# Performance work log

Hardware: AMD Instinct MI355X
Metric: run time of the kernel (lower is better)

The kernel has to match this reference:

```python
import jax, jax.numpy as jnp
import numpy as np

DEPTH, E, H, S, V, B = 6, 1024, 16, 2048, 32000, 2
HD = E // H
EPS = 1e-5


def _layernorm(x, w, b):
    mu = jnp.mean(x, axis=-1, keepdims=True)
    var = jnp.mean(jnp.square(x - mu), axis=-1, keepdims=True)
    return (x - mu) * jax.lax.rsqrt(var + EPS) * w + b


def setup_inputs() -> dict:
    key = jax.random.key(0)
    ks = jax.random.split(key, 8)
    std = 0.02
    return {
        "idx": jax.random.randint(ks[0], (B, S), 0, V),
        "tok_emb": jax.random.normal(ks[1], (V, E), jnp.float32) * std,
        "pos_emb": jax.random.normal(ks[2], (S, E), jnp.float32) * std,
        "qkv_w": jax.random.normal(ks[3], (DEPTH, 3 * E, E), jnp.float32) * std,
        "qkv_b": jnp.zeros((DEPTH, 3 * E), jnp.float32),
        "ln1_w": jnp.ones((DEPTH, E), jnp.float32),
        "ln1_b": jnp.zeros((DEPTH, E), jnp.float32),
        "ln2_w": jnp.ones((DEPTH, E), jnp.float32),
        "ln2_b": jnp.zeros((DEPTH, E), jnp.float32),
        "ff1_w": jax.random.normal(ks[4], (DEPTH, 4 * E, E), jnp.float32) * std,
        "ff1_b": jnp.zeros((DEPTH, 4 * E), jnp.float32),
        "ff2_w": jax.random.normal(ks[5], (DEPTH, E, 4 * E), jnp.float32) * std,
        "ff2_b": jnp.zeros((DEPTH, E), jnp.float32),
        "fin_w": jnp.ones((E,), jnp.float32),
        "fin_b": jnp.zeros((E,), jnp.float32),
        "proj_w": jax.random.normal(ks[6], (V, E), jnp.float32) * std,
    }


def _block(x, qkv_w, qkv_b, ln1_w, ln1_b, ln2_w, ln2_b, ff1_w, ff1_b, ff2_w, ff2_b):
    bs, seq, _ = x.shape
    # --- causal MSA (dropout in eval mode -> identity) ---
    xn = _layernorm(x, ln1_w, ln1_b)
    qkv = xn @ qkv_w.T + qkv_b                      # [B,S,3E]
    qkv = qkv.reshape(bs, seq, 3, H, HD)
    q, k, v = (jnp.moveaxis(qkv[:, :, i], 1, 2) for i in range(3))  # [B,H,S,HD]
    scores = jnp.einsum("bhqd,bhkd->bhqk", q, k) / jnp.sqrt(jnp.float32(HD))
    causal = jnp.triu(jnp.ones((seq, seq), bool), k=1)
    scores = jnp.where(causal[None, None], -jnp.inf, scores)
    probs = jax.nn.softmax(scores, axis=-1)
    attn = jnp.einsum("bhqk,bhkd->bqhd", probs, v).reshape(bs, seq, E)
    x = x + attn
    # --- feedforward ---
    xn = _layernorm(x, ln2_w, ln2_b)
    h = jax.nn.gelu(xn @ ff1_w.T + ff1_b, approximate=False)
    x = x + (h @ ff2_w.T + ff2_b)
    return x


def reference(idx, tok_emb, pos_emb, qkv_w, qkv_b, ln1_w, ln1_b, ln2_w, ln2_b,
              ff1_w, ff1_b, ff2_w, ff2_b, fin_w, fin_b, proj_w):
    bs, seq = idx.shape
    x = tok_emb[idx] + pos_emb[jnp.arange(seq)][None]  # [B,S,E]
    for l in range(DEPTH):
        x = _block(x, qkv_w[l], qkv_b[l], ln1_w[l], ln1_b[l], ln2_w[l], ln2_b[l],
                   ff1_w[l], ff1_b[l], ff2_w[l], ff2_b[l])
    x = _layernorm(x, fin_w, fin_b)
    logits = x @ proj_w.T  # [B,S,V], final_proj has no bias
    return logits
```

## Files before the change

### kernel.cpp

```cpp
#include <hip/hip_runtime.h>
#include <hip/hip_bf16.h>

#define DEPTH 6
#define E 1024
#define H 16
#define S 2048
#define V 32000
#define BB 2
#define HD 64
#define NTOK (BB * S)

typedef __attribute__((ext_vector_type(8))) short bf16x8;
typedef __attribute__((ext_vector_type(4))) float f32x4;
typedef unsigned short us;

__device__ inline us f2bf(float f) {
    union { float f; unsigned u; } v; v.f = f;
    unsigned r = v.u + 0x7fff + ((v.u >> 16) & 1);
    return (us)(r >> 16);
}
__device__ inline float bf2f(us b) {
    union { unsigned u; float f; } v; v.u = ((unsigned)b) << 16;
    return v.f;
}

__device__ __forceinline__ void gld16(const us* g, us* l) {
    __builtin_amdgcn_global_load_lds(
        (const __attribute__((address_space(1))) unsigned int*)g,
        (__attribute__((address_space(3))) unsigned int*)l, 16, 0, 0);
}

__global__ __launch_bounds__(256) void cast_kernel(const float* __restrict__ in,
                                                   us* __restrict__ out, int n8) {
    int i = blockIdx.x * 256 + threadIdx.x;
    if (i >= n8) return;
    const float4* p = (const float4*)in + 2 * (size_t)i;
    float4 a = p[0], b = p[1];
    uint4 o;
    o.x = f2bf(a.x) | ((unsigned)f2bf(a.y) << 16);
    o.y = f2bf(a.z) | ((unsigned)f2bf(a.w) << 16);
    o.z = f2bf(b.x) | ((unsigned)f2bf(b.y) << 16);
    o.w = f2bf(b.z) | ((unsigned)f2bf(b.w) << 16);
    ((uint4*)out)[i] = o;
}

__global__ void embed_kernel(const int* __restrict__ idx, const float* __restrict__ tok,
                             const float* __restrict__ pos, float* __restrict__ x) {
    int t = blockIdx.x;
    int s = t & (S - 1);
    int tokid = idx[t];
    int c = threadIdx.x * 4;
    float4 a = *(const float4*)&tok[(size_t)tokid * E + c];
    float4 p = *(const float4*)&pos[(size_t)s * E + c];
    float4 o; o.x = a.x + p.x; o.y = a.y + p.y; o.z = a.z + p.z; o.w = a.w + p.w;
    *(float4*)&x[(size_t)t * E + c] = o;
}

__global__ __launch_bounds__(256) void ln_kernel(const float* __restrict__ x,
                                                 const float* __restrict__ w,
                                                 const float* __restrict__ b,
                                                 us* __restrict__ out) {
    int row = blockIdx.x;
    int tid = threadIdx.x;
    int c = tid * 4;
    float4 v = *(const float4*)&x[(size_t)row * E + c];
    float s  = v.x + v.y + v.z + v.w;
    float sq = v.x * v.x + v.y * v.y + v.z * v.z + v.w * v.w;
    __shared__ float red[8];
    for (int o = 32; o > 0; o >>= 1) { s += __shfl_xor(s, o); sq += __shfl_xor(sq, o); }
    int wave = tid >> 6, lane = tid & 63;
    if (lane == 0) { red[wave] = s; red[4 + wave] = sq; }
    __syncthreads();
    if (tid == 0) {
        red[0] = red[0] + red[1] + red[2] + red[3];
        red[4] = red[4] + red[5] + red[6] + red[7];
    }
    __syncthreads();
    float mean = red[0] * (1.0f / E);
    float var  = red[4] * (1.0f / E) - mean * mean;
    float rstd = rsqrtf(var + 1e-5f);
    float4 wv = *(const float4*)&w[c];
    float4 bv = *(const float4*)&b[c];
    unsigned a0 = f2bf((v.x - mean) * rstd * wv.x + bv.x);
    unsigned a1 = f2bf((v.y - mean) * rstd * wv.y + bv.y);
    unsigned a2 = f2bf((v.z - mean) * rstd * wv.z + bv.z);
    unsigned a3 = f2bf((v.w - mean) * rstd * wv.w + bv.w);
    uint2 o; o.x = a0 | (a1 << 16); o.y = a2 | (a3 << 16);
    *(uint2*)&out[(size_t)row * E + c] = o;
}

__global__ __launch_bounds__(256) void combine_ln(const us* __restrict__ p0,
                                                  const us* __restrict__ p1,
                                                  const float* __restrict__ bias,
                                                  float* __restrict__ x,
                                                  const float* __restrict__ w,
                                                  const float* __restrict__ b,
                                                  us* __restrict__ out) {
    int row = blockIdx.x;
    int tid = threadIdx.x;
    int c = tid * 4;
    size_t base = (size_t)row * E + c;
    float4 v = *(const float4*)&x[base];
    uint2 a = *(const uint2*)&p0[base];
    uint2 bb2 = *(const uint2*)&p1[base];
    float4 bi = *(const float4*)&bias[c];
    v.x += bf2f((us)(a.x & 0xffff)) + bf2f((us)(bb2.x & 0xffff)) + bi.x;
    v.y += bf2f((us)(a.x >> 16))    + bf2f((us)(bb2.x >> 16))    + bi.y;
    v.z += bf2f((us)(a.y & 0xffff)) + bf2f((us)(bb2.y & 0xffff)) + bi.z;
    v.w += bf2f((us)(a.y >> 16))    + bf2f((us)(bb2.y >> 16))    + bi.w;
    *(float4*)&x[base] = v;

    float s  = v.x + v.y + v.z + v.w;
    float sq = v.x * v.x + v.y * v.y + v.z * v.z + v.w * v.w;
    __shared__ float red[8];
    for (int o = 32; o > 0; o >>= 1) { s += __shfl_xor(s, o); sq += __shfl_xor(sq, o); }
    int wave = tid >> 6, lane = tid & 63;
    if (lane == 0) { red[wave] = s; red[4 + wave] = sq; }
    __syncthreads();
    if (tid == 0) {
        red[0] = red[0] + red[1] + red[2] + red[3];
        red[4] = red[4] + red[5] + red[6] + red[7];
    }
    __syncthreads();
    float mean = red[0] * (1.0f / E);
    float var  = red[4] * (1.0f / E) - mean * mean;
    float rstd = rsqrtf(var + 1e-5f);
    float4 wv = *(const float4*)&w[c];
    float4 bv = *(const float4*)&b[c];
    unsigned a0 = f2bf((v.x - mean) * rstd * wv.x + bv.x);
    unsigned a1 = f2bf((v.y - mean) * rstd * wv.y + bv.y);
    unsigned a2 = f2bf((v.z - mean) * rstd * wv.z + bv.z);
    unsigned a3 = f2bf((v.w - mean) * rstd * wv.w + bv.w);
    uint2 o; o.x = a0 | (a1 << 16); o.y = a2 | (a3 << 16);
    *(uint2*)&out[base] = o;
}

#define GPH(dd, fb, STAGE, ISVM, IS12)                                              \
  {                                                                                 \
    bf16x8 afr0[2], afr1[2];                                                        \
    if ((fb) == 0) {                                                                \
      _Pragma("unroll")                                                             \
      for (int n = 0; n < 4; n++)                                                   \
        _Pragma("unroll")                                                           \
        for (int ks = 0; ks < 2; ks++)                                              \
          bfr[n][ks] = *(const bf16x8*)&lds[32768 + (dd) * 16384 +                  \
              (brow + n * 16) * 64 + ((ks * 4 + g4) ^ xg) * 8];                     \
    }                                                                               \
    _Pragma("unroll")                                                               \
    for (int ks = 0; ks < 2; ks++) {                                                \
      afr0[ks] = *(const bf16x8*)&lds[(dd) * 16384 + ((fb) >> 1) * 4096 +           \
          arow0 * 64 + ((ks * 4 + g4) ^ xg) * 8];                                   \
      afr1[ks] = *(const bf16x8*)&lds[(dd) * 16384 + ((fb) >> 1) * 4096 +           \
          arow1 * 64 + ((ks * 4 + g4) ^ xg) * 8];                                   \
    }                                                                               \
    STAGE;                                                                          \
    __builtin_amdgcn_sched_barrier(0);                                              \
    if (IS12) asm volatile("s_waitcnt lgkmcnt(8)" ::: "memory");                    \
    __builtin_amdgcn_s_barrier();                                                   \
    asm volatile("s_waitcnt lgkmcnt(0)" ::: "memory");                              \
    __builtin_amdgcn_sched_barrier(0);                                              \
    __builtin_amdgcn_s_setprio(1);                                                  \
    _Pragma("unroll")                                                               \
    for (int n = 0; n < 4; n++)                                                     \
      _Pragma("unroll")                                                             \
      for (int ks = 0; ks < 2; ks++) {                                              \
        acc[(fb)][n]     = __builtin_amdgcn_mfma_f32_16x16x32_bf16(afr0[ks], bfr[n][ks], acc[(fb)][n], 0, 0, 0);     \
        acc[(fb) + 1][n] = __builtin_amdgcn_mfma_f32_16x16x32_bf16(afr1[ks], bfr[n][ks], acc[(fb) + 1][n], 0, 0, 0); \
      }                                                                             \
    __builtin_amdgcn_s_setprio(0);                                                  \
    __builtin_amdgcn_sched_barrier(0);                                              \
    if (ISVM) asm volatile("s_waitcnt vmcnt(6)" ::: "memory");                      \
    __builtin_amdgcn_s_barrier();                                                   \
  }

template <int OUT_BF16, int ACT_GELU, int HAS_BIAS>
__global__ __launch_bounds__(512, 2) void gemm256(const us* __restrict__ A, int lda,
                                                  const us* __restrict__ Bw, int ldb,
                                                  const float* __restrict__ bias,
                                                  void* __restrict__ outp,
                                                  int M, int N, int K, int ldo) {
    __shared__ us lds[65536];
    int tid = threadIdx.x;
    int nwg = gridDim.x;
    int wgid = blockIdx.x;
    int chunk = nwg >> 3;
    int sw = (wgid & 7) * chunk + (wgid >> 3);
    int MB = M >> 8;
    int bm = (sw % MB) * 256;
    int bn = (sw / MB) * 256;
    int w = tid >> 6, lane = tid & 63;
    int wr = w >> 2, wc = w & 3;
    int l15 = lane & 15, g4 = lane >> 4;
    int xg = l15 & 7;
    int arow0 = (wr ? 32 : 0) + l15;
    int arow1 = arow0 + 16;
    int brow = wc * 64 + l15;
    int NT = K >> 6;

    f32x4 acc[8][4] = {};
    bf16x8 bfr[4][2];

    auto stA = [&](int u, int dd, int h) {
        int uu = (u < NT) ? u : NT - 1;
        #pragma unroll
        for (int i = 0; i < 2; i++) {
            int k = tid + i * 512;
            int q = 2 * h + (k >> 9);
            int r = (k >> 3) & 63;
            int tr = q * 32 + (r & 31) + ((r >> 5) << 7);
            int gp = (k & 7) ^ (r & 7);
            gld16(A + (size_t)(bm + tr) * lda + uu * 64 + gp * 8,
                  &lds[dd * 16384 + h * 8192 + k * 8]);
        }
    };
    auto stB = [&](int u, int dd, int h) {
        int uu = (u < NT) ? u : NT - 1;
        #pragma unroll
        for (int i = 0; i < 2; i++) {
            int k = tid + i * 512;
            int row = h * 128 + (k >> 3);
            int gp = (k & 7) ^ ((k >> 3) & 7);
            gld16(Bw + (size_t)(bn + row) * ldb + uu * 64 + gp * 8,
                  &lds[32768 + dd * 16384 + h * 8192 + k * 8]);
        }
    };

    stB(0, 0, 0); stB(0, 0, 1); stA(0, 0, 0); stA(0, 0, 1);
    stB(1, 1, 0); stB(1, 1, 1); stA(1, 1, 0);
    __builtin_amdgcn_sched_barrier(0);
    asm volatile("s_waitcnt vmcnt(6)" ::: "memory");
    __builtin_amdgcn_s_barrier();

    #pragma unroll 1
    for (int t = 0; t < NT; t += 2) {
        GPH(0, 0, stA(t + 1, 1, 1), 0, 1)
        GPH(0, 2, stB(t + 2, 0, 0), 0, 0)
        GPH(0, 4, stB(t + 2, 0, 1), 0, 0)
        GPH(0, 6, stA(t + 2, 0, 0), 1, 0)
        GPH(1, 0, stA(t + 2, 0, 1), 0, 1)
        GPH(1, 2, stB(t + 3, 1, 0), 0, 0)
        GPH(1, 4, stB(t + 3, 1, 1), 0, 0)
        GPH(1, 6, stA(t + 3, 1, 0), 1, 0)
    }

    float* outf = (float*)outp;
    us* outb = (us*)outp;
    #pragma unroll
    for (int mf = 0; mf < 8; mf++)
        #pragma unroll
        for (int n = 0; n < 4; n++)
            #pragma unroll
            for (int j = 0; j < 4; j++) {
                int r = bm + wr * 128 + mf * 16 + g4 * 4 + j;
                int c = bn + wc * 64 + n * 16 + l15;
                float v = acc[mf][n][j];
                if (HAS_BIAS) v += bias[c];
                if (ACT_GELU) v = 0.5f * v * (1.0f + erff(v * 0.70710678118f));
                if (OUT_BF16) outb[(size_t)r * ldo + c] = f2bf(v);
                else __builtin_nontemporal_store(v, &outf[(size_t)r * ldo + c]);
            }
}

template <int SPLITK>
__global__ __launch_bounds__(256) void gemm_bf16(const us* __restrict__ A, int lda,
                                                 const us* __restrict__ Bw, int ldb,
                                                 void* __restrict__ outp,
                                                 int M, int N, int K, int ldo) {
    __shared__ us As[2 * 128 * 32];
    __shared__ us Bs[2 * 128 * 32];
    int tid = threadIdx.x;
    int nwg = gridDim.x;
    int chunk = nwg >> 3;
    int wgid = blockIdx.x;
    int sw = (wgid & 7) * chunk + (wgid >> 3);

    int bm, bn;
    us* outb = (us*)outp;
    {
        int kz = sw >> 8;
        int rem = sw & 255;
        bm = (rem & 31) * 128;
        bn = (rem >> 5) * 128;
        A  += (size_t)kz * K;
        Bw += (size_t)kz * K;
        outb += (size_t)kz * M * ldo;
    }

    int wave = tid >> 6, lane = tid & 63;
    int wr = wave >> 1, wc = wave & 1;
    int l15 = lane & 15, g4 = lane >> 4;
    f32x4 acc[4][4] = {};

    for (int k0 = 0; k0 < K; k0 += 64) {
        #pragma unroll
        for (int p4 = 0; p4 < 4; p4++) {
            int p = p4 * 256 + tid;
            int ks = p >> 9, q = p & 511;
            int row = q >> 2, c8 = (q & 3) * 8;
            gld16(&A[(size_t)(bm + row) * lda + k0 + ks * 32 + c8], &As[p * 8]);
            gld16(&Bw[(size_t)(bn + row) * ldb + k0 + ks * 32 + c8], &Bs[p * 8]);
        }
        __syncthreads();
        bf16x8 a[4][2], bfr[4][2];
        #pragma unroll
        for (int m = 0; m < 4; m++)
            #pragma unroll
            for (int ks = 0; ks < 2; ks++)
                a[m][ks] = *(const bf16x8*)&As[ks * 4096 + (wr * 64 + m * 16 + l15) * 32 + g4 * 8];
        #pragma unroll
        for (int n = 0; n < 4; n++)
            #pragma unroll
            for (int ks = 0; ks < 2; ks++)
                bfr[n][ks] = *(const bf16x8*)&Bs[ks * 4096 + (wc * 64 + n * 16 + l15) * 32 + g4 * 8];
        #pragma unroll
        for (int m = 0; m < 4; m++)
            #pragma unroll
            for (int n = 0; n < 4; n++)
                #pragma unroll
                for (int ks = 0; ks < 2; ks++)
                    acc[m][n] = __builtin_amdgcn_mfma_f32_16x16x32_bf16(a[m][ks], bfr[n][ks], acc[m][n], 0, 0, 0);
        __syncthreads();
    }

    #pragma unroll
    for (int m = 0; m < 4; m++)
        #pragma unroll
        for (int n = 0; n < 4; n++)
            #pragma unroll
            for (int j = 0; j < 4; j++) {
                int r = bm + wr * 64 + m * 16 + g4 * 4 + j;
                int c = bn + wc * 64 + n * 16 + l15;
                outb[(size_t)r * ldo + c] = f2bf(acc[m][n][j]);
            }
}

__global__ __launch_bounds__(256) void transpose_v(const us* __restrict__ qkv,
                                                   us* __restrict__ vT) {
    int kt = blockIdx.x, h = blockIdx.y, b = blockIdx.z;
    int tid = threadIdx.x;
    __shared__ us T[64][72];
    const size_t base = (size_t)b * S * 3072 + 2048 + h * 64;
    int k0 = kt * 64;
    #pragma unroll
    for (int it = 0; it < 2; it++) {
        int p = tid + it * 256;
        int key = p & 63, c8 = (p >> 6) * 8;
        uint4 v = *(const uint4*)&qkv[base + (size_t)(k0 + key) * 3072 + c8];
        us* pv = (us*)&v;
        #pragma unroll
        for (int e = 0; e < 8; e++) T[c8 + e][key] = pv[e];
    }
    __syncthreads();
    const size_t obase = ((size_t)(b * H + h) * 64) * S + k0;
    #pragma unroll
    for (int it = 0; it < 2; it++) {
        int o = tid + it * 256;
        int d = o >> 3, cc = (o & 7) * 8;
        uint4 v = *(const uint4*)&T[d][cc];
        *(uint4*)&vT[obase + (size_t)d * S + cc] = v;
    }
}

__global__ __launch_bounds__(512, 4) void attn_kernel(const us* __restrict__ qkv,
                                                      const us* __restrict__ vT,
                                                      float* __restrict__ x) {
    int qt = blockIdx.x, h = blockIdx.y, b = blockIdx.z;
    int tid = threadIdx.x;
    int w = tid >> 6, lane = tid & 63;
    int l15 = lane & 15, g4 = lane >> 4;
    int s0 = qt * 128;
    int qrow_base = s0 + w * 16;
    const size_t qbase = (size_t)b * S * 3072;
    const size_t vtbase = ((size_t)(b * H + h) * 64) * S;

    __shared__ us K_lds[2][64 * 64];
    __shared__ us VT_lds[2][64 * 64];
    __shared__ us P_lds[8][16 * 72];

    bf16x8 q[2];
    #pragma unroll
    for (int dc = 0; dc < 2; dc++) {
        q[dc] = *(const bf16x8*)&qkv[qbase + (size_t)(qrow_base + l15) * 3072 + h * 64 + dc * 32 + 8 * g4];
        us* qq = (us*)&q[dc];
        #pragma unroll
        for (int e = 0; e < 8; e++) qq[e] = f2bf(bf2f(qq[e]) * 0.125f);
    }

    f32x4 O[4] = {};
    float m_run[4], l_run[4];
    #pragma unroll
    for (int j = 0; j < 4; j++) { m_run[j] = -INFINITY; l_run[j] = 0.0f; }

    int lastt = 2 * qt + 1;
    {
        int p = tid, row = p >> 3, cc = p & 7;
        int scc = cc ^ (row & 7);
        gld16(&qkv[qbase + (size_t)(0 + row) * 3072 + 1024 + h * 64 + scc * 8], &K_lds[0][p * 8]);
        gld16(&vT[vtbase + (size_t)row * S + 0 + scc * 8], &VT_lds[0][p * 8]);
    }
    __syncthreads();

    for (int t = 0; t <= lastt; t++) {
        int bb = t & 1;
        if (t < lastt) {
            int p = tid, row = p >> 3, cc = p & 7;
            int scc = cc ^ (row & 7);
            gld16(&qkv[qbase + (size_t)((t + 1) * 64 + row) * 3072 + 1024 + h * 64 + scc * 8], &K_lds[bb ^ 1][p * 8]);
            gld16(&vT[vtbase + (size_t)row * S + (t + 1) * 64 + scc * 8], &VT_lds[bb ^ 1][p * 8]);
        }
        int k0 = t * 64;
        if (k0 <= qrow_base + 15) {
            f32x4 sf[4];
            __builtin_amdgcn_s_setprio(1);
            #pragma unroll
            for (int c = 0; c < 4; c++) {
                f32x4 z = {};
                int row = c * 16 + l15;
                #pragma unroll
                for (int dc = 0; dc < 2; dc++) {
                    int ch = (dc * 4 + g4) ^ (row & 7);
                    bf16x8 kb = *(const bf16x8*)&K_lds[bb][row * 64 + ch * 8];
                    z = __builtin_amdgcn_mfma_f32_16x16x32_bf16(q[dc], kb, z, 0, 0, 0);
                }
                sf[c] = z;
            }
            __builtin_amdgcn_s_setprio(0);
            bool needmask = (k0 + 63 > qrow_base);
            float pr[4][4], alpha[4];
            #pragma unroll
            for (int j = 0; j < 4; j++) {
                int qrow = qrow_base + g4 * 4 + j;
                float v0 = sf[0][j], v1 = sf[1][j];
                float v2 = sf[2][j], v3 = sf[3][j];
                if (needmask) {
                    if (k0 +      l15 > qrow) v0 = -INFINITY;
                    if (k0 + 16 + l15 > qrow) v1 = -INFINITY;
                    if (k0 + 32 + l15 > qrow) v2 = -INFINITY;
                    if (k0 + 48 + l15 > qrow) v3 = -INFINITY;
                }
                float tm = fmaxf(fmaxf(v0, v1), fmaxf(v2, v3));
                tm = fmaxf(tm, __shfl_xor(tm, 1, 16));
                tm = fmaxf(tm, __shfl_xor(tm, 2, 16));
                tm = fmaxf(tm, __shfl_xor(tm, 4, 16));
                tm = fmaxf(tm, __shfl_xor(tm, 8, 16));
                float mnew = fmaxf(m_run[j], tm);
                float p0 = __expf(v0 - mnew), p1 = __expf(v1 - mnew);
                float p2 = __expf(v2 - mnew), p3 = __expf(v3 - mnew);
                float ts = (p0 + p1) + (p2 + p3);
                ts += __shfl_xor(ts, 1, 16);
                ts += __shfl_xor(ts, 2, 16);
                ts += __shfl_xor(ts, 4, 16);
                ts += __shfl_xor(ts, 8, 16);
                alpha[j] = __expf(m_run[j] - mnew);
                l_run[j] = l_run[j] * alpha[j] + ts;
                m_run[j] = mnew;
                pr[0][j] = p0; pr[1][j] = p1; pr[2][j] = p2; pr[3][j] = p3;
            }
            #pragma unroll
            for (int f = 0; f < 4; f++)
                #pragma unroll
                for (int j = 0; j < 4; j++) O[f][j] *= alpha[j];
            us* Pw = &P_lds[w][0];
            #pragma unroll
            for (int c = 0; c < 4; c++)
                #pragma unroll
                for (int j = 0; j < 4; j++)
                    Pw[(g4 * 4 + j) * 72 + c * 16 + l15] = f2bf(pr[c][j]);
            __builtin_amdgcn_s_setprio(1);
            #pragma unroll
            for (int kc = 0; kc < 2; kc++) {
                bf16x8 pa = *(const bf16x8*)&Pw[l15 * 72 + kc * 32 + g4 * 8];
                #pragma unroll
                for (int dt = 0; dt < 4; dt++) {
                    int row = dt * 16 + l15;
                    int ch = (kc * 4 + g4) ^ (row & 7);
                    bf16x8 vb = *(const bf16x8*)&VT_lds[bb][row * 64 + ch * 8];
                    O[dt] = __builtin_amdgcn_mfma_f32_16x16x32_bf16(pa, vb, O[dt], 0, 0, 0);
                }
            }
            __builtin_amdgcn_s_setprio(0);
        }
        __syncthreads();
    }
    #pragma unroll
    for (int dt = 0; dt < 4; dt++)
        #pragma unroll
        for (int j = 0; j < 4; j++) {
            size_t o = ((size_t)b * S + qrow_base + g4 * 4 + j) * E + h * 64 + dt * 16 + l15;
            x[o] += O[dt][j] / l_run[j];
        }
}

extern "C" void kernel_launch(void* const* d_in, const int* in_sizes, int n_in,
                              void* d_out, int out_size, void* d_ws, size_t ws_size,
                              hipStream_t stream) {
    const int*   idx    = (const int*)d_in[0];
    const float* tok    = (const float*)d_in[1];
    const float* pos    = (const float*)d_in[2];
    const float* qkv_w  = (const float*)d_in[3];
    const float* qkv_b  = (const float*)d_in[4];
    const float* ln1_w  = (const float*)d_in[5];
    const float* ln1_b  = (const float*)d_in[6];
    const float* ln2_w  = (const float*)d_in[7];
    const float* ln2_b  = (const float*)d_in[8];
    const float* ff1_w  = (const float*)d_in[9];
    const float* ff1_b  = (const float*)d_in[10];
    const float* ff2_w  = (const float*)d_in[11];
    const float* ff2_b  = (const float*)d_in[12];
    const float* fin_w  = (const float*)d_in[13];
    const float* fin_b  = (const float*)d_in[14];
    const float* proj_w = (const float*)d_in[15];

    char* ws = (char*)d_ws;
    float* x    = (float*)ws;
    us*    xn   = (us*)(ws + 16777216);
    us*    qkvb = (us*)(ws + 25165824);
    us*    hbuf = (us*)(ws + 50331648);
    us*    wbuf = (us*)(ws + 83886080);
    us*    vTb  = (us*)(ws + 92274688);
    us*    pbuf = qkvb;

    embed_kernel<<<NTOK, 256, 0, stream>>>(idx, tok, pos, x);
    ln_kernel<<<NTOK, 256, 0, stream>>>(x, ln1_w, ln1_b, xn);
    for (int l = 0; l < DEPTH; l++) {
        cast_kernel<<<1536, 256, 0, stream>>>(qkv_w + (size_t)l * 3 * E * E, wbuf, 3 * E * E / 8);
        gemm256<1, 0, 1><<<192, 512, 0, stream>>>(
            xn, E, wbuf, E, qkv_b + l * 3 * E, qkvb, NTOK, 3 * E, E, 3 * E);
        transpose_v<<<dim3(S / 64, H, BB), 256, 0, stream>>>(qkvb, vTb);
        attn_kernel<<<dim3(S / 128, H, BB), 512, 0, stream>>>(qkvb, vTb, x);
        ln_kernel<<<NTOK, 256, 0, stream>>>(x, ln2_w + l * E, ln2_b + l * E, xn);
        cast_kernel<<<2048, 256, 0, stream>>>(ff1_w + (size_t)l * 4 * E * E, wbuf, 4 * E * E / 8);
        gemm256<1, 1, 1><<<256, 512, 0, stream>>>(
            xn, E, wbuf, E, ff1_b + l * 4 * E, hbuf, NTOK, 4 * E, E, 4 * E);
        cast_kernel<<<2048, 256, 0, stream>>>(ff2_w + (size_t)l * E * 4 * E, wbuf, 4 * E * E / 8);
        gemm_bf16<1><<<512, 256, 0, stream>>>(
            hbuf, 4 * E, wbuf, 4 * E, qkvb, NTOK, E, 2 * E, E);
        const float* nw = (l < DEPTH - 1) ? (ln1_w + (l + 1) * E) : fin_w;
        const float* nb = (l < DEPTH - 1) ? (ln1_b + (l + 1) * E) : fin_b;
        combine_ln<<<NTOK, 256, 0, stream>>>(qkvb, qkvb + (size_t)NTOK * E, ff2_b + l * E,
                                             x, nw, nb, xn);
    }
    cast_kernel<<<16000, 256, 0, stream>>>(proj_w, pbuf, V * E / 8);
    gemm256<0, 0, 0><<<1024, 512, 0, stream>>>(
        xn, E, pbuf, E, nullptr, d_out, NTOK, 16384, E, V);
    gemm256<0, 0, 0><<<976, 512, 0, stream>>>(
        xn, E, pbuf + (size_t)16384 * E, E, nullptr, (float*)d_out + 16384, NTOK, 15616, E, V);
}
```

Baseline: 1.941 ms.

## Run FF2 as 4-way split-K on the 256 GEMM; add lazy softmax rescaling

The FF2 projection moves off the simple 128-tile 2-way split-K GEMM and onto the pipelined 256-tile gemm256 kernel with 4-way split-K. Three partials go to qkvb and the fourth goes to the vT buffer, and combine_ln now sums four bf16 partials. Separately, attention skips the running-max update and the O rescale unless any row's tile max exceeds the running max by more than 8. The row sum is kept per lane and reduced once at the end. The FF2 change trades more partial-output traffic for better GEMM efficiency, and the lazy rescale relies on a bounded exp growth for numerical safety.

```diff
diff --git a/kernel.cpp b/kernel.cpp
--- a/kernel.cpp
+++ b/kernel.cpp
@@ -89,8 +89,8 @@
     *(uint2*)&out[(size_t)row * E + c] = o;
 }
 
-__global__ __launch_bounds__(256) void combine_ln(const us* __restrict__ p0,
-                                                  const us* __restrict__ p1,
+__global__ __launch_bounds__(256) void combine_ln(const us* __restrict__ p012,
+                                                  const us* __restrict__ p3,
                                                   const float* __restrict__ bias,
                                                   float* __restrict__ x,
                                                   const float* __restrict__ w,
@@ -100,14 +100,17 @@
     int tid = threadIdx.x;
     int c = tid * 4;
     size_t base = (size_t)row * E + c;
+    const size_t stride = (size_t)NTOK * E;
     float4 v = *(const float4*)&x[base];
-    uint2 a = *(const uint2*)&p0[base];
-    uint2 bb2 = *(const uint2*)&p1[base];
+    uint2 a0 = *(const uint2*)&p012[base];
+    uint2 a1 = *(const uint2*)&p012[base + stride];
+    uint2 a2 = *(const uint2*)&p012[base + 2 * stride];
+    uint2 a3 = *(const uint2*)&p3[base];
     float4 bi = *(const float4*)&bias[c];
-    v.x += bf2f((us)(a.x & 0xffff)) + bf2f((us)(bb2.x & 0xffff)) + bi.x;
-    v.y += bf2f((us)(a.x >> 16))    + bf2f((us)(bb2.x >> 16))    + bi.y;
-    v.z += bf2f((us)(a.y & 0xffff)) + bf2f((us)(bb2.y & 0xffff)) + bi.z;
-    v.w += bf2f((us)(a.y >> 16))    + bf2f((us)(bb2.y >> 16))    + bi.w;
+    v.x += bf2f((us)(a0.x & 0xffff)) + bf2f((us)(a1.x & 0xffff)) + bf2f((us)(a2.x & 0xffff)) + bf2f((us)(a3.x & 0xffff)) + bi.x;
+    v.y += bf2f((us)(a0.x >> 16))    + bf2f((us)(a1.x >> 16))    + bf2f((us)(a2.x >> 16))    + bf2f((us)(a3.x >> 16))    + bi.y;
+    v.z += bf2f((us)(a0.y & 0xffff)) + bf2f((us)(a1.y & 0xffff)) + bf2f((us)(a2.y & 0xffff)) + bf2f((us)(a3.y & 0xffff)) + bi.z;
+    v.w += bf2f((us)(a0.y >> 16))    + bf2f((us)(a1.y >> 16))    + bf2f((us)(a2.y >> 16))    + bf2f((us)(a3.y >> 16))    + bi.w;
     *(float4*)&x[base] = v;
 
     float s  = v.x + v.y + v.z + v.w;
@@ -127,11 +130,11 @@
     float rstd = rsqrtf(var + 1e-5f);
     float4 wv = *(const float4*)&w[c];
     float4 bv = *(const float4*)&b[c];
-    unsigned a0 = f2bf((v.x - mean) * rstd * wv.x + bv.x);
-    unsigned a1 = f2bf((v.y - mean) * rstd * wv.y + bv.y);
-    unsigned a2 = f2bf((v.z - mean) * rstd * wv.z + bv.z);
-    unsigned a3 = f2bf((v.w - mean) * rstd * wv.w + bv.w);
-    uint2 o; o.x = a0 | (a1 << 16); o.y = a2 | (a3 << 16);
+    unsigned b0 = f2bf((v.x - mean) * rstd * wv.x + bv.x);
+    unsigned b1 = f2bf((v.y - mean) * rstd * wv.y + bv.y);
+    unsigned b2 = f2bf((v.z - mean) * rstd * wv.z + bv.z);
+    unsigned b3 = f2bf((v.w - mean) * rstd * wv.w + bv.w);
+    uint2 o; o.x = b0 | (b1 << 16); o.y = b2 | (b3 << 16);
     *(uint2*)&out[base] = o;
 }
 
@@ -173,11 +176,12 @@
     __builtin_amdgcn_s_barrier();                                                   \
   }
 
-template <int OUT_BF16, int ACT_GELU, int HAS_BIAS>
+template <int OUT_BF16, int ACT_GELU, int HAS_BIAS, int SPLITK>
 __global__ __launch_bounds__(512, 2) void gemm256(const us* __restrict__ A, int lda,
                                                   const us* __restrict__ Bw, int ldb,
                                                   const float* __restrict__ bias,
                                                   void* __restrict__ outp,
+                                                  void* __restrict__ outp3,
                                                   int M, int N, int K, int ldo) {
     __shared__ us lds[65536];
     int tid = threadIdx.x;
@@ -186,8 +190,23 @@
     int chunk = nwg >> 3;
     int sw = (wgid & 7) * chunk + (wgid >> 3);
     int MB = M >> 8;
-    int bm = (sw % MB) * 256;
-    int bn = (sw / MB) * 256;
+    int bm, bn;
+    us* outb;
+    float* outf = (float*)outp;
+    if (SPLITK) {
+        int ntile = MB * (N >> 8);
+        int kz = sw / ntile;
+        int rem = sw % ntile;
+        bm = (rem % MB) * 256;
+        bn = (rem / MB) * 256;
+        A  += (size_t)kz * K;
+        Bw += (size_t)kz * K;
+        outb = (kz < 3) ? (us*)outp + (size_t)kz * M * ldo : (us*)outp3;
+    } else {
+        bm = (sw % MB) * 256;
+        bn = (sw / MB) * 256;
+        outb = (us*)outp;
+    }
     int w = tid >> 6, lane = tid & 63;
     int wr = w >> 2, wc = w & 3;
     int l15 = lane & 15, g4 = lane >> 4;
@@ -243,8 +262,6 @@
         GPH(1, 6, stA(t + 3, 1, 0), 1, 0)
     }
 
-    float* outf = (float*)outp;
-    us* outb = (us*)outp;
     #pragma unroll
     for (int mf = 0; mf < 8; mf++)
         #pragma unroll
@@ -261,79 +278,6 @@
             }
 }
 
-template <int SPLITK>
-__global__ __launch_bounds__(256) void gemm_bf16(const us* __restrict__ A, int lda,
-                                                 const us* __restrict__ Bw, int ldb,
-                                                 void* __restrict__ outp,
-                                                 int M, int N, int K, int ldo) {
-    __shared__ us As[2 * 128 * 32];
-    __shared__ us Bs[2 * 128 * 32];
-    int tid = threadIdx.x;
-    int nwg = gridDim.x;
-    int chunk = nwg >> 3;
-    int wgid = blockIdx.x;
-    int sw = (wgid & 7) * chunk + (wgid >> 3);
-
-    int bm, bn;
-    us* outb = (us*)outp;
-    {
-        int kz = sw >> 8;
-        int rem = sw & 255;
-        bm = (rem & 31) * 128;
-        bn = (rem >> 5) * 128;
-        A  += (size_t)kz * K;
-        Bw += (size_t)kz * K;
-        outb += (size_t)kz * M * ldo;
-    }
-
-    int wave = tid >> 6, lane = tid & 63;
-    int wr = wave >> 1, wc = wave & 1;
-    int l15 = lane & 15, g4 = lane >> 4;
-    f32x4 acc[4][4] = {};
-
-    for (int k0 = 0; k0 < K; k0 += 64) {
-        #pragma unroll
-        for (int p4 = 0; p4 < 4; p4++) {
-            int p = p4 * 256 + tid;
-            int ks = p >> 9, q = p & 511;
-            int row = q >> 2, c8 = (q & 3) * 8;
-            gld16(&A[(size_t)(bm + row) * lda + k0 + ks * 32 + c8], &As[p * 8]);
-            gld16(&Bw[(size_t)(bn + row) * ldb + k0 + ks * 32 + c8], &Bs[p * 8]);
-        }
-        __syncthreads();
-        bf16x8 a[4][2], bfr[4][2];
-        #pragma unroll
-        for (int m = 0; m < 4; m++)
-            #pragma unroll
-            for (int ks = 0; ks < 2; ks++)
-                a[m][ks] = *(const bf16x8*)&As[ks * 4096 + (wr * 64 + m * 16 + l15) * 32 + g4 * 8];
-        #pragma unroll
-        for (int n = 0; n < 4; n++)
-            #pragma unroll
-            for (int ks = 0; ks < 2; ks++)
-                bfr[n][ks] = *(const bf16x8*)&Bs[ks * 4096 + (wc * 64 + n * 16 + l15) * 32 + g4 * 8];
-        #pragma unroll
-        for (int m = 0; m < 4; m++)
-            #pragma unroll
-            for (int n = 0; n < 4; n++)
-                #pragma unroll
-                for (int ks = 0; ks < 2; ks++)
-                    acc[m][n] = __builtin_amdgcn_mfma_f32_16x16x32_bf16(a[m][ks], bfr[n][ks], acc[m][n], 0, 0, 0);
-        __syncthreads();
-    }
-
-    #pragma unroll
-    for (int m = 0; m < 4; m++)
-        #pragma unroll
-        for (int n = 0; n < 4; n++)
-            #pragma unroll
-            for (int j = 0; j < 4; j++) {
-                int r = bm + wr * 64 + m * 16 + g4 * 4 + j;
-                int c = bn + wc * 64 + n * 16 + l15;
-                outb[(size_t)r * ldo + c] = f2bf(acc[m][n][j]);
-            }
-}
-
 __global__ __launch_bounds__(256) void transpose_v(const us* __restrict__ qkv,
                                                    us* __restrict__ vT) {
     int kt = blockIdx.x, h = blockIdx.y, b = blockIdx.z;
@@ -387,9 +331,9 @@
     }
 
     f32x4 O[4] = {};
-    float m_run[4], l_run[4];
-    #pragma unroll
-    for (int j = 0; j < 4; j++) { m_run[j] = -INFINITY; l_run[j] = 0.0f; }
+    float m_run[4], l_part[4];
+    #pragma unroll
+    for (int j = 0; j < 4; j++) { m_run[j] = -INFINITY; l_part[j] = 0.0f; }
 
     int lastt = 2 * qt + 1;
     {
@@ -426,7 +370,7 @@
             }
             __builtin_amdgcn_s_setprio(0);
             bool needmask = (k0 + 63 > qrow_base);
-            float pr[4][4], alpha[4];
+            float vv[4][4], tmr[4];
             #pragma unroll
             for (int j = 0; j < 4; j++) {
                 int qrow = qrow_base + g4 * 4 + j;
@@ -443,23 +387,34 @@
                 tm = fmaxf(tm, __shfl_xor(tm, 2, 16));
                 tm = fmaxf(tm, __shfl_xor(tm, 4, 16));
                 tm = fmaxf(tm, __shfl_xor(tm, 8, 16));
-                float mnew = fmaxf(m_run[j], tm);
-                float p0 = __expf(v0 - mnew), p1 = __expf(v1 - mnew);
-                float p2 = __expf(v2 - mnew), p3 = __expf(v3 - mnew);
-                float ts = (p0 + p1) + (p2 + p3);
-                ts += __shfl_xor(ts, 1, 16);
-                ts += __shfl_xor(ts, 2, 16);
-                ts += __shfl_xor(ts, 4, 16);
-                ts += __shfl_xor(ts, 8, 16);
-                alpha[j] = __expf(m_run[j] - mnew);
-                l_run[j] = l_run[j] * alpha[j] + ts;
-                m_run[j] = mnew;
+                tmr[j] = tm;
+                vv[0][j] = v0; vv[1][j] = v1; vv[2][j] = v2; vv[3][j] = v3;
+            }
+            bool grow = (tmr[0] > m_run[0] + 8.0f) || (tmr[1] > m_run[1] + 8.0f) ||
+                        (tmr[2] > m_run[2] + 8.0f) || (tmr[3] > m_run[3] + 8.0f);
+            bool skip = !__any(grow);
+            float pr[4][4], alpha[4];
+            #pragma unroll
+            for (int j = 0; j < 4; j++) {
+                float mnew = skip ? m_run[j] : fmaxf(m_run[j], tmr[j]);
+                float p0 = __expf(vv[0][j] - mnew), p1 = __expf(vv[1][j] - mnew);
+                float p2 = __expf(vv[2][j] - mnew), p3 = __expf(vv[3][j] - mnew);
+                float sum4 = (p0 + p1) + (p2 + p3);
+                if (skip) {
+                    l_part[j] += sum4;
+                } else {
+                    alpha[j] = __expf(m_run[j] - mnew);
+                    l_part[j] = l_part[j] * alpha[j] + sum4;
+                    m_run[j] = mnew;
+                }
                 pr[0][j] = p0; pr[1][j] = p1; pr[2][j] = p2; pr[3][j] = p3;
             }
-            #pragma unroll
-            for (int f = 0; f < 4; f++)
+            if (!skip) {
                 #pragma unroll
-                for (int j = 0; j < 4; j++) O[f][j] *= alpha[j];
+                for (int f = 0; f < 4; f++)
+                    #pragma unroll
+                    for (int j = 0; j < 4; j++) O[f][j] *= alpha[j];
+            }
             us* Pw = &P_lds[w][0];
             #pragma unroll
             for (int c = 0; c < 4; c++)
@@ -482,6 +437,16 @@
         }
         __syncthreads();
     }
+    float l_run[4];
+    #pragma unroll
+    for (int j = 0; j < 4; j++) {
+        float l = l_part[j];
+        l += __shfl_xor(l, 1, 16);
+        l += __shfl_xor(l, 2, 16);
+        l += __shfl_xor(l, 4, 16);
+        l += __shfl_xor(l, 8, 16);
+        l_run[j] = l;
+    }
     #pragma unroll
     for (int dt = 0; dt < 4; dt++)
         #pragma unroll
@@ -524,25 +489,24 @@
     ln_kernel<<<NTOK, 256, 0, stream>>>(x, ln1_w, ln1_b, xn);
     for (int l = 0; l < DEPTH; l++) {
         cast_kernel<<<1536, 256, 0, stream>>>(qkv_w + (size_t)l * 3 * E * E, wbuf, 3 * E * E / 8);
-        gemm256<1, 0, 1><<<192, 512, 0, stream>>>(
-            xn, E, wbuf, E, qkv_b + l * 3 * E, qkvb, NTOK, 3 * E, E, 3 * E);
+        gemm256<1, 0, 1, 0><<<192, 512, 0, stream>>>(
+            xn, E, wbuf, E, qkv_b + l * 3 * E, qkvb, nullptr, NTOK, 3 * E, E, 3 * E);
         transpose_v<<<dim3(S / 64, H, BB), 256, 0, stream>>>(qkvb, vTb);
         attn_kernel<<<dim3(S / 128, H, BB), 512, 0, stream>>>(qkvb, vTb, x);
         ln_kernel<<<NTOK, 256, 0, stream>>>(x, ln2_w + l * E, ln2_b + l * E, xn);
         cast_kernel<<<2048, 256, 0, stream>>>(ff1_w + (size_t)l * 4 * E * E, wbuf, 4 * E * E / 8);
-        gemm256<1, 1, 1><<<256, 512, 0, stream>>>(
-            xn, E, wbuf, E, ff1_b + l * 4 * E, hbuf, NTOK, 4 * E, E, 4 * E);
+        gemm256<1, 1, 1, 0><<<256, 512, 0, stream>>>(
+            xn, E, wbuf, E, ff1_b + l * 4 * E, hbuf, nullptr, NTOK, 4 * E, E, 4 * E);
         cast_kernel<<<2048, 256, 0, stream>>>(ff2_w + (size_t)l * E * 4 * E, wbuf, 4 * E * E / 8);
-        gemm_bf16<1><<<512, 256, 0, stream>>>(
-            hbuf, 4 * E, wbuf, 4 * E, qkvb, NTOK, E, 2 * E, E);
+        gemm256<1, 0, 0, 1><<<256, 512, 0, stream>>>(
+            hbuf, 4 * E, wbuf, 4 * E, nullptr, qkvb, vTb, NTOK, E, E, E);
         const float* nw = (l < DEPTH - 1) ? (ln1_w + (l + 1) * E) : fin_w;
         const float* nb = (l < DEPTH - 1) ? (ln1_b + (l + 1) * E) : fin_b;
-        combine_ln<<<NTOK, 256, 0, stream>>>(qkvb, qkvb + (size_t)NTOK * E, ff2_b + l * E,
-                                             x, nw, nb, xn);
+        combine_ln<<<NTOK, 256, 0, stream>>>(qkvb, vTb, ff2_b + l * E, x, nw, nb, xn);
     }
     cast_kernel<<<16000, 256, 0, stream>>>(proj_w, pbuf, V * E / 8);
-    gemm256<0, 0, 0><<<1024, 512, 0, stream>>>(
-        xn, E, pbuf, E, nullptr, d_out, NTOK, 16384, E, V);
-    gemm256<0, 0, 0><<<976, 512, 0, stream>>>(
-        xn, E, pbuf + (size_t)16384 * E, E, nullptr, (float*)d_out + 16384, NTOK, 15616, E, V);
-}
+    gemm256<0, 0, 0, 0><<<1024, 512, 0, stream>>>(
+        xn, E, pbuf, E, nullptr, d_out, nullptr, NTOK, 16384, E, V);
+    gemm256<0, 0, 0, 0><<<976, 512, 0, stream>>>(
+        xn, E, pbuf + (size_t)16384 * E, E, nullptr, (float*)d_out + 16384, nullptr, NTOK, 15616, E, V);
+}
```

Measured after the change: 1.819 ms. 6.2% less time.
